# Optimization experiments

Hardware: AMD Instinct MI355X
Metric: run time of the kernel (lower is better)

## Reference

```python
import jax, jax.numpy as jnp
import numpy as np

EPS = 1e-8
NUM_HEADS = 8


def setup_inputs() -> dict:
    key = jax.random.key(0)
    ks = jax.random.split(key, 12)
    B, T, F = 8, 512, 512
    H = NUM_HEADS
    dh = F // H
    maxlen = 2048
    s = 0.02  # weight init scale
    inp = {
        "x": jax.random.normal(ks[0], (B, T, F), jnp.float32),
        "Wq": jax.random.normal(ks[1], (F, F), jnp.float32) * s,
        "bq": jax.random.normal(ks[2], (F,), jnp.float32) * s,
        "Wk": jax.random.normal(ks[3], (F, F), jnp.float32) * s,
        "bk": jax.random.normal(ks[4], (F,), jnp.float32) * s,
        "Wv": jax.random.normal(ks[5], (F, F), jnp.float32) * s,
        "bv": jax.random.normal(ks[6], (F,), jnp.float32) * s,
        "Wo": jax.random.normal(ks[7], (F, F), jnp.float32) * s,
        "bo": jax.random.normal(ks[8], (F,), jnp.float32) * s,
        "delta": jnp.ones((1,), jnp.float32),
        "cache_k": jax.random.normal(ks[9], (B * H, maxlen, dh), jnp.float32) * 0.1,
        "cache_v": jax.random.normal(ks[10], (B * H, maxlen, dh), jnp.float32) * 0.1,
    }
    return inp


def _split_heads(t, H):
    # torch.cat(torch.split(t, dh, dim=-1), dim=0): head index outermost on dim 0
    B, T, F = t.shape
    dh = F // H
    return t.reshape(B, T, H, dh).transpose(2, 0, 1, 3).reshape(H * B, T, dh)


def _merge_heads(t, H):
    HB, T, dh = t.shape
    B = HB // H
    return t.reshape(H, B, T, dh).transpose(1, 2, 0, 3).reshape(B, T, H * dh)


def reference(x, Wq, bq, Wk, bk, Wv, bv, Wo, bo, delta, cache_k, cache_v):
    B, T, F = x.shape
    H = NUM_HEADS
    maxlen = cache_k.shape[1]
    d = jnp.sqrt(jnp.asarray(F, jnp.float32))

    q = _split_heads(x @ Wq.T + bq, H)  # [H*B, T, dh]
    k = _split_heads(x @ Wk.T + bk, H)
    v = _split_heads(x @ Wv.T + bv, H)

    # rolling KV cache: drop oldest T, append new T -> length maxlen
    k_full = jnp.concatenate([cache_k[:, T:], k], axis=1)  # [H*B, maxlen, dh]
    v_full = jnp.concatenate([cache_v[:, T:], v], axis=1)

    # Gaussian positional bias G = exp(-(i-j)^2 / (delta^2 + EPS)), last T rows
    i = jnp.arange(maxlen, dtype=jnp.float32)
    ind = -(i[:, None] - i[None, :]) ** 2  # [maxlen, maxlen]
    G = jnp.exp(ind[-T:] / (delta[0] ** 2 + EPS))  # [T, maxlen]

    scores = jnp.abs(jnp.einsum('btd,bsd->bts', q, k_full) * G / d)
    attn = jax.nn.softmax(scores, axis=-1)  # [H*B, T, maxlen]
    o = jnp.einsum('bts,bsd->btd', attn, v_full)  # [H*B, T, dh]

    out = _merge_heads(o, H) @ Wo.T + bo  # [B, T, F]
    return out
```

## Files before the change

### kernel.cpp

```cpp
#include <hip/hip_runtime.h>
#include <cstdint>
#include <cstddef>


typedef _Float16 f16x8 __attribute__((ext_vector_type(8)));
typedef _Float16 f16x4 __attribute__((ext_vector_type(4)));
typedef float f32x4 __attribute__((ext_vector_type(4)));

#define GLOBAL_AS __attribute__((address_space(1)))
#define LDS_AS __attribute__((address_space(3)))

__launch_bounds__(256)
__global__ void prep(const float* __restrict__ x,
                     const float* __restrict__ Wq, const float* __restrict__ Wk,
                     const float* __restrict__ Wv, const float* __restrict__ Wo,
                     const float* __restrict__ cache_v,
                     _Float16* __restrict__ xh, _Float16* __restrict__ wh,
                     float* __restrict__ part) {
  const int bid = blockIdx.x;
  const int tid = threadIdx.x;
  if (bid < 2048) {
    long e = ((long)bid * 256 + tid) * 4;
    float4 v = *(const float4*)(x + e);
    f16x4 h;
    h[0] = (_Float16)v.x; h[1] = (_Float16)v.y;
    h[2] = (_Float16)v.z; h[3] = (_Float16)v.w;
    *(f16x4*)(xh + e) = h;
  } else if (bid < 3072) {
    long e = ((long)(bid - 2048) * 256 + tid) * 4;
    int seg = (int)(e >> 18);
    const float* w = seg == 0 ? Wq : seg == 1 ? Wk : seg == 2 ? Wv : Wo;
    float4 v = *(const float4*)(w + (e & 262143));
    f16x4 h;
    h[0] = (_Float16)v.x; h[1] = (_Float16)v.y;
    h[2] = (_Float16)v.z; h[3] = (_Float16)v.w;
    *(f16x4*)(wh + e) = h;
  } else {
    int pb = bid - 3072;
    int hb = pb >> 4, chunk = pb & 15;
    int g = tid & 15, p = tid >> 4;
    int r0 = 512 + chunk * 96;
    float4 s4 = {0.f, 0.f, 0.f, 0.f};
#pragma unroll
    for (int it = 0; it < 6; it++) {
      int r = r0 + p + it * 16;
      float4 v = *(const float4*)(cache_v + ((size_t)hb * 2048 + r) * 64 + g * 4);
      s4.x += v.x; s4.y += v.y; s4.z += v.z; s4.w += v.w;
    }
    __shared__ float4 red4[256];
    red4[tid] = s4;
    __syncthreads();
    if (tid < 64) {
      int gg = tid >> 2, c = tid & 3;
      float s = 0.f;
#pragma unroll
      for (int p2 = 0; p2 < 16; p2++) {
        float4 v = red4[p2 * 16 + gg];
        s += (c == 0) ? v.x : (c == 1) ? v.y : (c == 2) ? v.z : v.w;
      }
      part[(hb * 16 + chunk) * 64 + tid] = s;
    }
  }
}

__launch_bounds__(256)
__global__ void gemm_qkv(const _Float16* __restrict__ xh,
                         const _Float16* __restrict__ wh,
                         const float* __restrict__ bq,
                         const float* __restrict__ bk,
                         const float* __restrict__ bv,
                         _Float16* __restrict__ q, _Float16* __restrict__ k,
                         _Float16* __restrict__ v,
                         float* __restrict__ svnewp) {
  __shared__ __align__(16) _Float16 As[4 * 128 * 32];
  __shared__ __align__(16) _Float16 Bs[4 * 64 * 32];
  const int tid = threadIdx.x;
  const int bid = blockIdx.x;
  const int swz = (bid & 7) * 96 + (bid >> 3);
  const int bx = swz / 24;
  const int by = swz - bx * 24;
  const int m0 = bx * 128;
  const int n0g = by * 64;
  const int which = n0g >> 9;
  const int nloc0 = n0g & 511;
  const _Float16* Bsel = wh + (size_t)which * 262144;
  const float* bsel = which == 0 ? bq : which == 1 ? bk : bv;
  _Float16* osel = which == 0 ? q : which == 1 ? k : v;
  const int w = tid >> 6, lane = tid & 63;
  const int c16 = lane & 15, q4 = lane >> 4;
  const int wm = (w & 1) * 64, wn = (w >> 1) * 32;

  f32x4 acc[4][2];
#pragma unroll
  for (int i = 0; i < 4; i++)
#pragma unroll
    for (int j = 0; j < 2; j++) acc[i][j] = (f32x4){0.f, 0.f, 0.f, 0.f};

  for (int k0 = 0; k0 < 512; k0 += 128) {
    __syncthreads();
#pragma unroll
    for (int it = 0; it < 8; it++) {
      int c = it * 256 + tid;
      int sub = c >> 9, row = (c >> 2) & 127, c8 = (c & 3) * 8;
      __builtin_amdgcn_global_load_lds(
          (const GLOBAL_AS void*)(xh + (size_t)(m0 + row) * 512 + k0 + sub * 32 + c8),
          (LDS_AS void*)(As + c * 8), 16, 0, 0);
    }
#pragma unroll
    for (int it = 0; it < 4; it++) {
      int c = it * 256 + tid;
      int sub = c >> 8, row = (c >> 2) & 63, c8 = (c & 3) * 8;
      __builtin_amdgcn_global_load_lds(
          (const GLOBAL_AS void*)(Bsel + (size_t)(nloc0 + row) * 512 + k0 + sub * 32 + c8),
          (LDS_AS void*)(Bs + c * 8), 16, 0, 0);
    }
    __syncthreads();

#pragma unroll
    for (int sub = 0; sub < 4; sub++) {
      f16x8 af[4], bf[2];
#pragma unroll
      for (int i = 0; i < 4; i++)
        af[i] = *(const f16x8*)(As + sub * 4096 + (wm + i * 16 + c16) * 32 + q4 * 8);
#pragma unroll
      for (int j = 0; j < 2; j++)
        bf[j] = *(const f16x8*)(Bs + sub * 2048 + (wn + j * 16 + c16) * 32 + q4 * 8);
#pragma unroll
      for (int i = 0; i < 4; i++)
#pragma unroll
        for (int j = 0; j < 2; j++)
          acc[i][j] = __builtin_amdgcn_mfma_f32_16x16x32_f16(af[i], bf[j], acc[i][j], 0, 0, 0);
    }
  }

  const int mbase = m0 + wm + (q4 << 2);
  const int nbase = nloc0 + wn + c16;
  float cs[2] = {0.f, 0.f};
#pragma unroll
  for (int i = 0; i < 4; i++)
#pragma unroll
    for (int j = 0; j < 2; j++) {
      int fg = nbase + j * 16;
      float bv2 = bsel[fg];
      int h = fg >> 6, dd = fg & 63;
#pragma unroll
      for (int r = 0; r < 4; r++) {
        int m = mbase + i * 16 + r;
        int b = m >> 9, t = m & 511;
        float val = acc[i][j][r] + bv2;
        osel[(((size_t)((h << 3) + b) * 512 + t) << 6) + dd] = (_Float16)val;
        cs[j] += val;
      }
    }
  if (which == 2) {
    const int b = m0 >> 9;
    const int slot = ((m0 + wm) >> 6) & 7;
#pragma unroll
    for (int j = 0; j < 2; j++) {
      cs[j] += __shfl_xor(cs[j], 16, 64);
      cs[j] += __shfl_xor(cs[j], 32, 64);
      if (q4 == 0) {
        int fg = nbase + j * 16;
        int h = fg >> 6, dd = fg & 63;
        svnewp[((slot << 6) + ((h << 3) + b)) * 64 + dd] = cs[j];
      }
    }
  }
}

__launch_bounds__(256)
__global__ void attn_mfma(const _Float16* __restrict__ q,
                          const _Float16* __restrict__ k_new,
                          const _Float16* __restrict__ v_new,
                          const float* __restrict__ cache_k,
                          const float* __restrict__ cache_v,
                          const float* __restrict__ part,
                          const float* __restrict__ svnewp,
                          const float* __restrict__ delta,
                          _Float16* __restrict__ o_merged) {
  const int lin = blockIdx.y * 8 + blockIdx.x;
  const int swz = (lin & 7) * 64 + (lin >> 3);
  const int hb = swz >> 3;
  const int t0 = (swz & 7) * 64;
  const int jlo_t = 1520 + t0;

  __shared__ __align__(16) _Float16 Q_sh[64 * 72];
  __shared__ __align__(16) _Float16 K_sh[96 * 72];
  __shared__ __align__(16) _Float16 VT_sh[64 * 104];
  __shared__ __align__(16) _Float16 P_sh[64 * 104];
  __shared__ float G_sh[40];
  __shared__ float id_sh[64], sv_sh[64];

  const int tid = threadIdx.x;
  const int w = tid >> 6, lane = tid & 63;
  const float dscale = 0.044194173824159216f;

  if (tid < 36) {
    int di = tid - 16;
    float inv_g = 1.0f / (delta[0] * delta[0] + 1e-8f);
    G_sh[tid] = (tid <= 32) ? expf(-(float)(di * di) * inv_g) : 0.f;
  }
  if (tid >= 64 && tid < 128) {
    int d = tid - 64;
    float s = 0.f;
#pragma unroll
    for (int sl = 0; sl < 8; sl++) s += svnewp[((sl << 6) + hb) * 64 + d];
#pragma unroll
    for (int c = 0; c < 16; c++) s += part[(hb * 16 + c) * 64 + d];
    sv_sh[d] = s;
  }
#pragma unroll
  for (int it = 0; it < 2; it++) {
    int idx = it * 256 + tid;
    int r = idx >> 3, c8 = (idx & 7) * 8;
    *(f16x8*)(Q_sh + r * 72 + c8) =
        *(const f16x8*)(q + ((size_t)hb * 512 + t0 + r) * 64 + c8);
  }
  f16x4 vreg[6];
#pragma unroll
  for (int it = 0; it < 6; it++) {
    int idx = it * 256 + tid;
    int r = idx >> 4, c4 = idx & 15;
    int j = jlo_t + r;
    f16x4 kh, vh;
    if (j < 1536) {
      float4 k4 = *(const float4*)(cache_k + ((size_t)hb * 2048 + j + 512) * 64 + c4 * 4);
      float4 v4 = *(const float4*)(cache_v + ((size_t)hb * 2048 + j + 512) * 64 + c4 * 4);
      kh[0] = (_Float16)k4.x; kh[1] = (_Float16)k4.y;
      kh[2] = (_Float16)k4.z; kh[3] = (_Float16)k4.w;
      vh[0] = (_Float16)v4.x; vh[1] = (_Float16)v4.y;
      vh[2] = (_Float16)v4.z; vh[3] = (_Float16)v4.w;
    } else if (j < 2048) {
      kh = *(const f16x4*)(k_new + ((size_t)hb * 512 + (j - 1536)) * 64 + c4 * 4);
      vh = *(const f16x4*)(v_new + ((size_t)hb * 512 + (j - 1536)) * 64 + c4 * 4);
    } else {
#pragma unroll
      for (int e = 0; e < 4; e++) { kh[e] = (_Float16)0.f; vh[e] = (_Float16)0.f; }
    }
    *(f16x4*)(K_sh + r * 72 + c4 * 4) = kh;
    vreg[it] = vh;
  }
  asm volatile("s_waitcnt lgkmcnt(0)" ::: "memory");
  __builtin_amdgcn_s_barrier();

  {
    const int c16 = lane & 15;
    const int q4 = lane >> 4;
    const int koff = q4 * 8;
    const int mrow = w * 16 + c16;
    f16x8 aq0 = *(const f16x8*)(Q_sh + mrow * 72 + koff);
    f16x8 aq1 = *(const f16x8*)(Q_sh + mrow * 72 + 32 + koff);
    f32x4 accS[3];
#pragma unroll
    for (int n2 = 0; n2 < 3; n2++) accS[n2] = (f32x4){0.f, 0.f, 0.f, 0.f};
    __builtin_amdgcn_s_setprio(1);
#pragma unroll
    for (int n2 = 0; n2 < 3; n2++) {
      int n = w + n2;
      f16x8 b0 = *(const f16x8*)(K_sh + (n * 16 + c16) * 72 + koff);
      f16x8 b1 = *(const f16x8*)(K_sh + (n * 16 + c16) * 72 + 32 + koff);
      accS[n2] = __builtin_amdgcn_mfma_f32_16x16x32_f16(aq0, b0, accS[n2], 0, 0, 0);
      accS[n2] = __builtin_amdgcn_mfma_f32_16x16x32_f16(aq1, b1, accS[n2], 0, 0, 0);
    }
    __builtin_amdgcn_s_setprio(0);
    const int jmax = 527 - t0;
    float sum_r[4] = {0.f, 0.f, 0.f, 0.f};
#pragma unroll
    for (int n2 = 0; n2 < 3; n2++) {
      int jb = (w + n2) * 16 + c16;
#pragma unroll
      for (int r = 0; r < 4; r++) {
        int row = w * 16 + q4 * 4 + r;
        int off = jb - row;
        bool valid = (off >= 0) && (off <= 32) && (jb <= jmax);
        int offc = min(max(off, 0), 32);
        float g = G_sh[offc];
        float val = fabsf(accS[n2][r]) * dscale * g;
        float wgt = valid ? (expf(val) - 1.0f) : 0.f;
        sum_r[r] += wgt;
        P_sh[row * 104 + jb] = (_Float16)wgt;
      }
    }
    {
      int zt = w + 3 - ((w & 1) << 2);
      int jb = zt * 16 + c16;
#pragma unroll
      for (int r = 0; r < 4; r++)
        P_sh[(w * 16 + q4 * 4 + r) * 104 + jb] = (_Float16)0.f;
    }
#pragma unroll
    for (int r = 0; r < 4; r++) {
#pragma unroll
      for (int mk = 1; mk < 16; mk <<= 1)
        sum_r[r] += __shfl_xor(sum_r[r], mk, 64);
      if (c16 == 0) {
        int row = w * 16 + q4 * 4 + r;
        id_sh[row] = 1.0f / (sum_r[r] + 2048.f);
      }
    }
  }

#pragma unroll
  for (int it = 0; it < 6; it++) {
    int idx = it * 256 + tid;
    int r = idx >> 4, c4 = idx & 15;
    f16x4 vh = vreg[it];
#pragma unroll
    for (int e = 0; e < 4; e++) VT_sh[(c4 * 4 + e) * 104 + r] = vh[e];
  }
  __syncthreads();

  f32x4 accO[4];
#pragma unroll
  for (int mi = 0; mi < 4; mi++) accO[mi] = (f32x4){0.f, 0.f, 0.f, 0.f};
  {
    const int koff = (lane >> 4) * 8;
    const int nrow = w * 16 + (lane & 15);
    f16x8 bv0 = *(const f16x8*)(VT_sh + nrow * 104 + 0 + koff);
    f16x8 bv1 = *(const f16x8*)(VT_sh + nrow * 104 + 32 + koff);
    f16x8 bv2 = *(const f16x8*)(VT_sh + nrow * 104 + 64 + koff);
    __builtin_amdgcn_s_setprio(1);
#pragma unroll
    for (int mi = 0; mi < 4; mi++) {
      const int kc = mi >> 1;
      f16x8 bva = (kc == 0) ? bv0 : bv1;
      f16x8 bvb = (kc == 0) ? bv1 : bv2;
      f16x8 apa = *(const f16x8*)(P_sh + (mi * 16 + (lane & 15)) * 104 + kc * 32 + koff);
      accO[mi] = __builtin_amdgcn_mfma_f32_16x16x32_f16(apa, bva, accO[mi], 0, 0, 0);
      f16x8 apb = *(const f16x8*)(P_sh + (mi * 16 + (lane & 15)) * 104 + (kc + 1) * 32 + koff);
      accO[mi] = __builtin_amdgcn_mfma_f32_16x16x32_f16(apb, bvb, accO[mi], 0, 0, 0);
    }
    __builtin_amdgcn_s_setprio(0);
  }

  const int h = hb >> 3, b = hb & 7;
  const int d = w * 16 + (lane & 15);
  const float svd = sv_sh[d];
#pragma unroll
  for (int mi = 0; mi < 4; mi++)
#pragma unroll
    for (int r = 0; r < 4; r++) {
      int trow = mi * 16 + ((lane >> 4) << 2) + r;
      float val = (accO[mi][r] + svd) * id_sh[trow];
      o_merged[((size_t)(b * 512 + t0 + trow)) * 512 + h * 64 + d] = (_Float16)val;
    }
}

__launch_bounds__(256)
__global__ void gemm_out(const _Float16* __restrict__ A,
                         const _Float16* __restrict__ Bw,
                         const float* __restrict__ bias,
                         float* __restrict__ out) {
  __shared__ __align__(16) _Float16 As[4 * 64 * 32];
  __shared__ __align__(16) _Float16 Bs[4 * 64 * 32];
  const int tid = threadIdx.x;
  const int bid = blockIdx.x;
  const int swz = (bid & 7) * 64 + (bid >> 3);
  const int m0 = (swz >> 3) * 64;
  const int n0 = (swz & 7) * 64;
  const int w = tid >> 6, lane = tid & 63;
  const int c16 = lane & 15, q4 = lane >> 4;
  const int wm = (w & 1) * 32, wn = (w >> 1) * 32;

  f32x4 acc[2][2];
#pragma unroll
  for (int i = 0; i < 2; i++)
#pragma unroll
    for (int j = 0; j < 2; j++) acc[i][j] = (f32x4){0.f, 0.f, 0.f, 0.f};

  for (int k0 = 0; k0 < 512; k0 += 128) {
    __syncthreads();
#pragma unroll
    for (int it = 0; it < 4; it++) {
      int c = it * 256 + tid;
      int sub = c >> 8, row = (c >> 2) & 63, c8 = (c & 3) * 8;
      __builtin_amdgcn_global_load_lds(
          (const GLOBAL_AS void*)(A + (size_t)(m0 + row) * 512 + k0 + sub * 32 + c8),
          (LDS_AS void*)(As + c * 8), 16, 0, 0);
      __builtin_amdgcn_global_load_lds(
          (const GLOBAL_AS void*)(Bw + (size_t)(n0 + row) * 512 + k0 + sub * 32 + c8),
          (LDS_AS void*)(Bs + c * 8), 16, 0, 0);
    }
    __syncthreads();

#pragma unroll
    for (int sub = 0; sub < 4; sub++) {
      f16x8 af[2], bf[2];
#pragma unroll
      for (int i = 0; i < 2; i++)
        af[i] = *(const f16x8*)(As + sub * 2048 + (wm + i * 16 + c16) * 32 + q4 * 8);
#pragma unroll
      for (int j = 0; j < 2; j++)
        bf[j] = *(const f16x8*)(Bs + sub * 2048 + (wn + j * 16 + c16) * 32 + q4 * 8);
#pragma unroll
      for (int i = 0; i < 2; i++)
#pragma unroll
        for (int j = 0; j < 2; j++)
          acc[i][j] = __builtin_amdgcn_mfma_f32_16x16x32_f16(af[i], bf[j], acc[i][j], 0, 0, 0);
    }
  }

  const int mbase = m0 + wm + (q4 << 2);
  const int nbase = n0 + wn + c16;
#pragma unroll
  for (int i = 0; i < 2; i++)
#pragma unroll
    for (int j = 0; j < 2; j++) {
      int fg = nbase + j * 16;
      float bv = bias[fg];
#pragma unroll
      for (int r = 0; r < 4; r++) {
        int m = mbase + i * 16 + r;
        out[(size_t)m * 512 + fg] = acc[i][j][r] + bv;
      }
    }
}

extern "C" void kernel_launch(void* const* d_in, const int* in_sizes, int n_in,
                              void* d_out, int out_size, void* d_ws, size_t ws_size,
                              hipStream_t stream) {
  const float* x = (const float*)d_in[0];
  const float* Wq = (const float*)d_in[1];
  const float* bq = (const float*)d_in[2];
  const float* Wk = (const float*)d_in[3];
  const float* bk = (const float*)d_in[4];
  const float* Wv = (const float*)d_in[5];
  const float* bv = (const float*)d_in[6];
  const float* Wo = (const float*)d_in[7];
  const float* bo = (const float*)d_in[8];
  const float* delta = (const float*)d_in[9];
  const float* cache_k = (const float*)d_in[10];
  const float* cache_v = (const float*)d_in[11];
  float* out = (float*)d_out;

  _Float16* xh = (_Float16*)d_ws;
  _Float16* wh = xh + 2097152;
  _Float16* qf = wh + 1048576;
  _Float16* kf = qf + 2097152;
  _Float16* vf = kf + 2097152;
  float* part = (float*)(vf + 2097152);
  float* svnewp = part + 65536;
  _Float16* oh = (_Float16*)(svnewp + 32768);

  prep<<<4096, 256, 0, stream>>>(x, Wq, Wk, Wv, Wo, cache_v, xh, wh, part);

  gemm_qkv<<<768, 256, 0, stream>>>(xh, wh, bq, bk, bv, qf, kf, vf, svnewp);
  gemm_qkv<<<768, 256, 0, stream>>>(xh, wh, bq, bk, bv, qf, kf, vf, svnewp);
  gemm_qkv<<<768, 256, 0, stream>>>(xh, wh, bq, bk, bv, qf, kf, vf, svnewp);

  dim3 g2(8, 64);
  attn_mfma<<<g2, 256, 0, stream>>>(qf, kf, vf, cache_k, cache_v, part, svnewp,
                                    delta, oh);

  gemm_out<<<512, 256, 0, stream>>>(oh, wh + 3 * 262144, bo, out);
}
```

Baseline: 170.3 us.

## Drop redundant QKV GEMM launches, move cache_v partial sums into GEMM grid

```diff
diff --git a/kernel.cpp b/kernel.cpp
--- a/kernel.cpp
+++ b/kernel.cpp
@@ -14,9 +14,7 @@
 __global__ void prep(const float* __restrict__ x,
                      const float* __restrict__ Wq, const float* __restrict__ Wk,
                      const float* __restrict__ Wv, const float* __restrict__ Wo,
-                     const float* __restrict__ cache_v,
-                     _Float16* __restrict__ xh, _Float16* __restrict__ wh,
-                     float* __restrict__ part) {
+                     _Float16* __restrict__ xh, _Float16* __restrict__ wh) {
   const int bid = blockIdx.x;
   const int tid = threadIdx.x;
   if (bid < 2048) {
@@ -26,7 +24,7 @@
     h[0] = (_Float16)v.x; h[1] = (_Float16)v.y;
     h[2] = (_Float16)v.z; h[3] = (_Float16)v.w;
     *(f16x4*)(xh + e) = h;
-  } else if (bid < 3072) {
+  } else {
     long e = ((long)(bid - 2048) * 256 + tid) * 4;
     int seg = (int)(e >> 18);
     const float* w = seg == 0 ? Wq : seg == 1 ? Wk : seg == 2 ? Wv : Wo;
@@ -35,31 +33,6 @@
     h[0] = (_Float16)v.x; h[1] = (_Float16)v.y;
     h[2] = (_Float16)v.z; h[3] = (_Float16)v.w;
     *(f16x4*)(wh + e) = h;
-  } else {
-    int pb = bid - 3072;
-    int hb = pb >> 4, chunk = pb & 15;
-    int g = tid & 15, p = tid >> 4;
-    int r0 = 512 + chunk * 96;
-    float4 s4 = {0.f, 0.f, 0.f, 0.f};
-#pragma unroll
-    for (int it = 0; it < 6; it++) {
-      int r = r0 + p + it * 16;
-      float4 v = *(const float4*)(cache_v + ((size_t)hb * 2048 + r) * 64 + g * 4);
-      s4.x += v.x; s4.y += v.y; s4.z += v.z; s4.w += v.w;
-    }
-    __shared__ float4 red4[256];
-    red4[tid] = s4;
-    __syncthreads();
-    if (tid < 64) {
-      int gg = tid >> 2, c = tid & 3;
-      float s = 0.f;
-#pragma unroll
-      for (int p2 = 0; p2 < 16; p2++) {
-        float4 v = red4[p2 * 16 + gg];
-        s += (c == 0) ? v.x : (c == 1) ? v.y : (c == 2) ? v.z : v.w;
-      }
-      part[(hb * 16 + chunk) * 64 + tid] = s;
-    }
   }
 }
 
@@ -69,13 +42,44 @@
                          const float* __restrict__ bq,
                          const float* __restrict__ bk,
                          const float* __restrict__ bv,
+                         const float* __restrict__ cache_v,
                          _Float16* __restrict__ q, _Float16* __restrict__ k,
                          _Float16* __restrict__ v,
-                         float* __restrict__ svnewp) {
+                         float* __restrict__ svnewp,
+                         float* __restrict__ part) {
   __shared__ __align__(16) _Float16 As[4 * 128 * 32];
   __shared__ __align__(16) _Float16 Bs[4 * 64 * 32];
   const int tid = threadIdx.x;
   const int bid = blockIdx.x;
+
+  if (bid >= 768) {
+    int pb = bid - 768;
+    int hb = pb >> 4, chunk = pb & 15;
+    int g = tid & 15, p = tid >> 4;
+    int r0 = 512 + chunk * 96;
+    float4 s4 = {0.f, 0.f, 0.f, 0.f};
+#pragma unroll
+    for (int it = 0; it < 6; it++) {
+      int r = r0 + p + it * 16;
+      float4 vv = *(const float4*)(cache_v + ((size_t)hb * 2048 + r) * 64 + g * 4);
+      s4.x += vv.x; s4.y += vv.y; s4.z += vv.z; s4.w += vv.w;
+    }
+    float4* red4 = (float4*)As;
+    red4[tid] = s4;
+    __syncthreads();
+    if (tid < 64) {
+      int gg = tid >> 2, c = tid & 3;
+      float s = 0.f;
+#pragma unroll
+      for (int p2 = 0; p2 < 16; p2++) {
+        float4 vv = red4[p2 * 16 + gg];
+        s += (c == 0) ? vv.x : (c == 1) ? vv.y : (c == 2) ? vv.z : vv.w;
+      }
+      part[(hb * 16 + chunk) * 64 + tid] = s;
+    }
+    return;
+  }
+
   const int swz = (bid & 7) * 96 + (bid >> 3);
   const int bx = swz / 24;
   const int by = swz - bx * 24;
@@ -184,7 +188,6 @@
   const int t0 = (swz & 7) * 64;
   const int jlo_t = 1520 + t0;
 
-  __shared__ __align__(16) _Float16 Q_sh[64 * 72];
   __shared__ __align__(16) _Float16 K_sh[96 * 72];
   __shared__ __align__(16) _Float16 VT_sh[64 * 104];
   __shared__ __align__(16) _Float16 P_sh[64 * 104];
@@ -195,6 +198,12 @@
   const int w = tid >> 6, lane = tid & 63;
   const float dscale = 0.044194173824159216f;
 
+  const int c16e = lane & 15;
+  const int q4e = lane >> 4;
+  const int mrow = w * 16 + c16e;
+  f16x8 aq0 = *(const f16x8*)(q + ((size_t)hb * 512 + t0 + mrow) * 64 + q4e * 8);
+  f16x8 aq1 = *(const f16x8*)(q + ((size_t)hb * 512 + t0 + mrow) * 64 + 32 + q4e * 8);
+
   if (tid < 36) {
     int di = tid - 16;
     float inv_g = 1.0f / (delta[0] * delta[0] + 1e-8f);
@@ -208,13 +217,6 @@
 #pragma unroll
     for (int c = 0; c < 16; c++) s += part[(hb * 16 + c) * 64 + d];
     sv_sh[d] = s;
-  }
-#pragma unroll
-  for (int it = 0; it < 2; it++) {
-    int idx = it * 256 + tid;
-    int r = idx >> 3, c8 = (idx & 7) * 8;
-    *(f16x8*)(Q_sh + r * 72 + c8) =
-        *(const f16x8*)(q + ((size_t)hb * 512 + t0 + r) * 64 + c8);
   }
   f16x4 vreg[6];
 #pragma unroll
@@ -247,9 +249,6 @@
     const int c16 = lane & 15;
     const int q4 = lane >> 4;
     const int koff = q4 * 8;
-    const int mrow = w * 16 + c16;
-    f16x8 aq0 = *(const f16x8*)(Q_sh + mrow * 72 + koff);
-    f16x8 aq1 = *(const f16x8*)(Q_sh + mrow * 72 + 32 + koff);
     f32x4 accS[3];
 #pragma unroll
     for (int n2 = 0; n2 < 3; n2++) accS[n2] = (f32x4){0.f, 0.f, 0.f, 0.f};
@@ -442,11 +441,10 @@
   float* svnewp = part + 65536;
   _Float16* oh = (_Float16*)(svnewp + 32768);
 
-  prep<<<4096, 256, 0, stream>>>(x, Wq, Wk, Wv, Wo, cache_v, xh, wh, part);
-
-  gemm_qkv<<<768, 256, 0, stream>>>(xh, wh, bq, bk, bv, qf, kf, vf, svnewp);
-  gemm_qkv<<<768, 256, 0, stream>>>(xh, wh, bq, bk, bv, qf, kf, vf, svnewp);
-  gemm_qkv<<<768, 256, 0, stream>>>(xh, wh, bq, bk, bv, qf, kf, vf, svnewp);
+  prep<<<3072, 256, 0, stream>>>(x, Wq, Wk, Wv, Wo, xh, wh);
+
+  gemm_qkv<<<1792, 256, 0, stream>>>(xh, wh, bq, bk, bv, cache_v,
+                                     qf, kf, vf, svnewp, part);
 
   dim3 g2(8, 64);
   attn_mfma<<<g2, 256, 0, stream>>>(qf, kf, vf, cache_k, cache_v, part, svnewp,
```

Measured after the change: 147.7 us. 1.15x faster.
